# Performance work log

Measured on AMD Instinct MI355X. Metric: run time of the kernel, lower is better.

The kernel has to match this reference:

```python
import jax, jax.numpy as jnp
import numpy as np
import math

BS, QL, KL = 2, 2048, 2048
H, D = 16, 64          # n_heads, cell_dim
QS = KS = VS = 1024    # query/key/value feature sizes
HD = H * D


def setup_inputs() -> dict:
    key = jax.random.key(0)
    ks = jax.random.split(key, 12)
    s_in = 1.0 / math.sqrt(QS)
    s_hd = 1.0 / math.sqrt(HD)
    return {
        "query": jax.random.normal(ks[0], (BS, QL, QS), jnp.float32),
        "key": jax.random.normal(ks[1], (BS, KL, KS), jnp.float32),
        "value": jax.random.normal(ks[2], (BS, KL, VS), jnp.float32),
        # nn.Linear weights stored as [in, out] for x @ W + b
        "Wq_w": jax.random.normal(ks[3], (QS, HD), jnp.float32) * s_in,
        "Wq_b": jax.random.normal(ks[4], (HD,), jnp.float32) * s_in,
        "Wk_w": jax.random.normal(ks[5], (KS, HD), jnp.float32) * s_in,
        "Wk_b": jax.random.normal(ks[6], (HD,), jnp.float32) * s_in,
        "Wv_w": jax.random.normal(ks[7], (VS, HD), jnp.float32) * s_in,
        "Wv_b": jax.random.normal(ks[8], (HD,), jnp.float32) * s_in,
        "Wo_w": jax.random.normal(ks[9], (HD, HD), jnp.float32) * s_hd,
        "Wo_b": jax.random.normal(ks[10], (HD,), jnp.float32) * s_hd,
    }


def reference(query, key, value, Wq_w, Wq_b, Wk_w, Wk_b, Wv_w, Wv_b, Wo_w, Wo_b):
    bs, ql, _ = query.shape
    kl = key.shape[1]
    # project and split heads; torch .chunk along dim 2 == head-major reshape
    q = (query @ Wq_w + Wq_b).reshape(bs, ql, H, D).transpose(0, 2, 1, 3)  # bhqd
    k = (key @ Wk_w + Wk_b).reshape(bs, kl, H, D).transpose(0, 2, 1, 3)    # bhkd
    v = (value @ Wv_w + Wv_b).reshape(bs, kl, H, D).transpose(0, 2, 1, 3)  # bhkd
    scores = jnp.einsum("bhqd,bhkd->bhqk", q, k) / jnp.sqrt(jnp.float32(D))
    # log_softmax(...).exp() == softmax (use_mask=False path)
    w = jax.nn.softmax(scores, axis=-1)
    heads = jnp.einsum("bhqk,bhkd->bhqd", w, v)
    out = heads.transpose(0, 2, 1, 3).reshape(bs, ql, HD)  # concat heads on dim 2
    return out @ Wo_w + Wo_b
```

## Files before the change

kernel.cpp:

```cpp
#include <hip/hip_runtime.h>

#define BSZ 2
#define SEQ 2048
#define NH 16
#define DHD 64
#define HDIM 1024
#define FS 1024
#define MR (BSZ*SEQ)
#define L2E 1.4426950408889634f

typedef __bf16 bf16x8 __attribute__((ext_vector_type(8)));
typedef __bf16 bf16x2t __attribute__((ext_vector_type(2)));
typedef float f32x4 __attribute__((ext_vector_type(4)));
typedef float f32x16 __attribute__((ext_vector_type(16)));
typedef unsigned short u16;
typedef unsigned int u32;
typedef u32 u32x4 __attribute__((ext_vector_type(4)));

__device__ __forceinline__ u16 f2bf(float f) {
  u32 x = __float_as_uint(f);
  return (u16)((x + 0x7fffu + ((x >> 16) & 1u)) >> 16);
}

__device__ __forceinline__ u32 pack2bf(float a, float b) {
  bf16x2t t = {(__bf16)a, (__bf16)b};
  return __builtin_bit_cast(u32, t);
}

__device__ __forceinline__ void gload16(const void* g, void* l) {
  __builtin_amdgcn_global_load_lds(
      (const __attribute__((address_space(1))) u32*)g,
      (__attribute__((address_space(3))) u32*)l, 16, 0, 0);
}

__global__ __launch_bounds__(256) void cast3_k(const float* __restrict__ q,
                                               const float* __restrict__ k,
                                               const float* __restrict__ v,
                                               u16* __restrict__ dst, int n4) {
  int i = blockIdx.x * 256 + threadIdx.x;
  const int st = gridDim.x * 256;
  const int tot = 3 * n4;
  for (; i < tot; i += st) {
    const int arr = i >> 20;
    const int idx = i & (n4 - 1);
    const float* src = arr == 0 ? q : arr == 1 ? k : v;
    float4 vv = ((const float4*)src)[idx];
    ushort4 o;
    o.x = f2bf(vv.x); o.y = f2bf(vv.y); o.z = f2bf(vv.z); o.w = f2bf(vv.w);
    ((ushort4*)dst)[i] = o;
  }
}

__global__ __launch_bounds__(256) void transw4_k(
    const float* __restrict__ W0, const float* __restrict__ W1,
    const float* __restrict__ W2, const float* __restrict__ W3,
    u16* __restrict__ WTbase) {
  __shared__ float t[32][33];
  const int z = blockIdx.z;
  const float* W = z == 0 ? W0 : z == 1 ? W1 : z == 2 ? W2 : W3;
  u16* WT = WTbase + (size_t)z * FS * HDIM;
  const int tx = threadIdx.x, ty = threadIdx.y;
  const int c0 = blockIdx.x * 32, r0 = blockIdx.y * 32;
#pragma unroll
  for (int i = 0; i < 4; i++)
    t[ty + 8 * i][tx] = W[(size_t)(r0 + ty + 8 * i) * FS + c0 + tx];
  __syncthreads();
#pragma unroll
  for (int i = 0; i < 4; i++)
    WT[(size_t)(c0 + ty + 8 * i) * FS + r0 + tx] = f2bf(t[tx][ty + 8 * i]);
}

__global__ __launch_bounds__(256, 2) void gemmQKV_k(
    const u16* __restrict__ Abase, const u16* __restrict__ WTbase,
    const float* __restrict__ bq, const float* __restrict__ bk,
    const float* __restrict__ bv, u16* __restrict__ QKbase,
    u16* __restrict__ VpT) {
  __shared__ u16 aL[128 * 64];
  __shared__ u16 bL[128 * 64];
  const int grp = blockIdx.y;
  const u16* A = Abase + (size_t)grp * MR * FS;
  const u16* BT = WTbase + (size_t)grp * FS * HDIM;
  const float* bias = grp == 0 ? bq : grp == 1 ? bk : bv;
  const int m0 = (blockIdx.x >> 3) << 7;
  const int n0 = (blockIdx.x & 7) << 7;
  const int tid = threadIdx.x, w = tid >> 6, lane = tid & 63;
  const int wr = ((w >> 1) << 6), wc = ((w & 1) << 6);
  const int li = lane & 15, g = lane >> 4;

  f32x4 acc[4][4];
#pragma unroll
  for (int i = 0; i < 4; i++)
#pragma unroll
    for (int j = 0; j < 4; j++) acc[i][j] = (f32x4){0.f, 0.f, 0.f, 0.f};

  for (int k0 = 0; k0 < FS; k0 += 64) {
#pragma unroll
    for (int j = 0; j < 4; j++) {
      const int c = w * 4 + j;
      const int r = c * 8 + (lane >> 3);
      const int sc = (lane & 7) ^ (r & 7);
      gload16(A + (size_t)(m0 + r) * FS + k0 + sc * 8, (char*)aL + c * 1024);
      gload16(BT + (size_t)(n0 + r) * FS + k0 + sc * 8, (char*)bL + c * 1024);
    }
    __syncthreads();
    bf16x8 af[2][4], bfr[2][4];
#pragma unroll
    for (int ks = 0; ks < 2; ks++) {
#pragma unroll
      for (int mf = 0; mf < 4; mf++) {
        const int r = wr + mf * 16 + li;
        const int sl = (g + 4 * ks) ^ (r & 7);
        af[ks][mf] = *(const bf16x8*)((const char*)aL + r * 128 + sl * 16);
      }
#pragma unroll
      for (int nf = 0; nf < 4; nf++) {
        const int r = wc + nf * 16 + li;
        const int sl = (g + 4 * ks) ^ (r & 7);
        bfr[ks][nf] = *(const bf16x8*)((const char*)bL + r * 128 + sl * 16);
      }
    }
#pragma unroll
    for (int ks = 0; ks < 2; ks++)
#pragma unroll
      for (int mf = 0; mf < 4; mf++)
#pragma unroll
        for (int nf = 0; nf < 4; nf++)
          acc[mf][nf] = __builtin_amdgcn_mfma_f32_16x16x32_bf16(
              af[ks][mf], bfr[ks][nf], acc[mf][nf], 0, 0, 0);
    __syncthreads();
  }

  if (grp < 2) {
    const float osc = grp == 0 ? 0.125f * L2E : 1.0f;
    u16* C = QKbase + (size_t)grp * MR * HDIM;
#pragma unroll
    for (int mf = 0; mf < 4; mf++)
#pragma unroll
      for (int nf = 0; nf < 4; nf++) {
        const int n = n0 + wc + nf * 16 + li;
        const float bvl = bias[n];
#pragma unroll
        for (int r4 = 0; r4 < 4; r4++) {
          const int m = m0 + wr + mf * 16 + g * 4 + r4;
          C[(size_t)m * HDIM + n] = f2bf((acc[mf][nf][r4] + bvl) * osc);
        }
      }
  } else {
#pragma unroll
    for (int mf = 0; mf < 4; mf++)
#pragma unroll
      for (int nf = 0; nf < 4; nf++) {
        const int n = n0 + wc + nf * 16 + li;
        const float bvl = bias[n];
        const int m = m0 + wr + mf * 16 + g * 4;
        const int bb = m >> 11, kv = m & 2047;
        ushort4 o;
        o.x = f2bf(acc[mf][nf][0] + bvl);
        o.y = f2bf(acc[mf][nf][1] + bvl);
        o.z = f2bf(acc[mf][nf][2] + bvl);
        o.w = f2bf(acc[mf][nf][3] + bvl);
        *(ushort4*)(VpT +
                    ((size_t)(bb * NH + (n >> 6)) * DHD + (n & 63)) * SEQ + kv) = o;
      }
  }
}

__global__ __launch_bounds__(256, 2) void gemm_out_k(
    const u16* __restrict__ A, const u16* __restrict__ BT,
    const float* __restrict__ bias, float* __restrict__ C) {
  __shared__ u16 aL[128 * 64];
  __shared__ u16 bL[128 * 64];
  const int m0 = (blockIdx.x >> 3) << 7;
  const int n0 = (blockIdx.x & 7) << 7;
  const int tid = threadIdx.x, w = tid >> 6, lane = tid & 63;
  const int wr = ((w >> 1) << 6), wc = ((w & 1) << 6);
  const int li = lane & 15, g = lane >> 4;

  f32x4 acc[4][4];
#pragma unroll
  for (int i = 0; i < 4; i++)
#pragma unroll
    for (int j = 0; j < 4; j++) acc[i][j] = (f32x4){0.f, 0.f, 0.f, 0.f};

  for (int k0 = 0; k0 < HDIM; k0 += 64) {
#pragma unroll
    for (int j = 0; j < 4; j++) {
      const int c = w * 4 + j;
      const int r = c * 8 + (lane >> 3);
      const int sc = (lane & 7) ^ (r & 7);
      gload16(A + (size_t)(m0 + r) * HDIM + k0 + sc * 8, (char*)aL + c * 1024);
      gload16(BT + (size_t)(n0 + r) * HDIM + k0 + sc * 8, (char*)bL + c * 1024);
    }
    __syncthreads();
    bf16x8 af[2][4], bfr[2][4];
#pragma unroll
    for (int ks = 0; ks < 2; ks++) {
#pragma unroll
      for (int mf = 0; mf < 4; mf++) {
        const int r = wr + mf * 16 + li;
        const int sl = (g + 4 * ks) ^ (r & 7);
        af[ks][mf] = *(const bf16x8*)((const char*)aL + r * 128 + sl * 16);
      }
#pragma unroll
      for (int nf = 0; nf < 4; nf++) {
        const int r = wc + nf * 16 + li;
        const int sl = (g + 4 * ks) ^ (r & 7);
        bfr[ks][nf] = *(const bf16x8*)((const char*)bL + r * 128 + sl * 16);
      }
    }
#pragma unroll
    for (int ks = 0; ks < 2; ks++)
#pragma unroll
      for (int mf = 0; mf < 4; mf++)
#pragma unroll
        for (int nf = 0; nf < 4; nf++)
          acc[mf][nf] = __builtin_amdgcn_mfma_f32_16x16x32_bf16(
              af[ks][mf], bfr[ks][nf], acc[mf][nf], 0, 0, 0);
    __syncthreads();
  }

#pragma unroll
  for (int mf = 0; mf < 4; mf++)
#pragma unroll
    for (int nf = 0; nf < 4; nf++) {
      const int n = n0 + wc + nf * 16 + li;
      const float bvl = bias[n];
#pragma unroll
      for (int r4 = 0; r4 < 4; r4++) {
        const int m = m0 + wr + mf * 16 + g * 4 + r4;
        C[(size_t)m * HDIM + n] = acc[mf][nf][r4] + bvl;
      }
    }
}

__global__ __launch_bounds__(512, 1) void attn_k(
    const u16* __restrict__ Qp, const u16* __restrict__ Kp,
    const u16* __restrict__ VpT, u16* __restrict__ Hd) {
  __shared__ u16 kbuf[4][64 * 64];
  __shared__ u16 vbuf[4][64 * 64];

  const int bid = blockIdx.x;
  const int swz = (bid & 7) * 64 + (bid >> 3);
  const int qb = swz & 15;
  const int h = (swz >> 4) & 15;
  const int b = swz >> 8;
  const int tid = threadIdx.x, w = tid >> 6, lane = tid & 63;
  const int sel = w >> 2, g3 = w & 3;
  const int q32 = lane & 31, hi = lane >> 5;
  const int q0 = qb << 7;
  const size_t qbase = (size_t)(b * SEQ + q0) * HDIM + (size_t)h * DHD;
  const size_t kbase = (size_t)(b * SEQ) * HDIM + (size_t)h * DHD;
  const size_t vtbase = (size_t)(b * NH + h) * DHD * SEQ;

  const int rr = lane >> 3;
  const int sc8 = ((lane & 7) ^ rr) * 8;
  const int fkey = (q32 & 7) << 4;

#pragma unroll
  for (int j = 0; j < 2; j++) {
    const int c = w * 2 + j;
    const int r = c * 8 + rr;
    gload16(Qp + qbase + (size_t)r * HDIM + sc8, (char*)kbuf + c * 1024);
  }
  __syncthreads();
  bf16x8 qf[4];
  {
    const char* qbp = (const char*)kbuf + (g3 * 32 + q32) * 128;
#pragma unroll
    for (int ds = 0; ds < 4; ds++)
      qf[ds] = *(const bf16x8*)(qbp + ((32 * ds + 16 * hi) ^ fkey));
  }
  __syncthreads();

  float mrun = -1e30f, lrun = 0.f;
  f32x16 o0, o1;
#pragma unroll
  for (int i = 0; i < 16; i++) { o0[i] = 0.f; o1[i] = 0.f; }

  auto stagePair = [&](int tp) {
    const int t = tp + sel;
    const int buf = t & 3;
    const size_t kb = kbase + (size_t)(t * 64) * HDIM;
    const size_t vb = vtbase + (size_t)(t * 64);
#pragma unroll
    for (int j = 0; j < 2; j++) {
      const int c = g3 * 2 + j;
      const int r = c * 8 + rr;
      gload16(Kp + kb + (size_t)r * HDIM + sc8, (char*)kbuf[buf] + c * 1024);
      gload16(VpT + vb + (size_t)r * SEQ + sc8, (char*)vbuf[buf] + c * 1024);
    }
  };

  stagePair(0);

#pragma unroll 1
  for (int p = 0; p < SEQ / 128; p++) {
    __syncthreads();
    if (p + 1 < SEQ / 128) stagePair(2 * p + 2);
    const int t = 2 * p + sel;
    const char* kl = (const char*)kbuf[t & 3];
    const char* vl = (const char*)vbuf[t & 3];

    f32x16 s0, s1;
#pragma unroll
    for (int i = 0; i < 16; i++) { s0[i] = 0.f; s1[i] = 0.f; }
#pragma unroll
    for (int ds = 0; ds < 4; ds++) {
      const int off = (32 * ds + 16 * hi) ^ fkey;
      const bf16x8 ka = *(const bf16x8*)(kl + q32 * 128 + off);
      const bf16x8 kb2 = *(const bf16x8*)(kl + (32 + q32) * 128 + off);
      s0 = __builtin_amdgcn_mfma_f32_32x32x16_bf16(ka, qf[ds], s0, 0, 0, 0);
      s1 = __builtin_amdgcn_mfma_f32_32x32x16_bf16(kb2, qf[ds], s1, 0, 0, 0);
    }

    float mt[16];
#pragma unroll
    for (int i = 0; i < 16; i++) mt[i] = fmaxf(s0[i], s1[i]);
#pragma unroll
    for (int i = 0; i < 8; i++) mt[i] = fmaxf(mt[i], mt[i + 8]);
#pragma unroll
    for (int i = 0; i < 4; i++) mt[i] = fmaxf(mt[i], mt[i + 4]);
    float mx = fmaxf(fmaxf(mt[0], mt[1]), fmaxf(mt[2], mt[3]));
    mx = fmaxf(mx, __shfl_xor(mx, 32));
    if (!__all(mx <= mrun + 8.0f)) {
      const float mnew = fmaxf(mrun, mx);
      const float scl = __builtin_amdgcn_exp2f(mrun - mnew);
      mrun = mnew;
      lrun *= scl;
#pragma unroll
      for (int i = 0; i < 16; i++) { o0[i] *= scl; o1[i] *= scl; }
    }
    float p0[16], p1[16];
#pragma unroll
    for (int i = 0; i < 16; i++) {
      p0[i] = __builtin_amdgcn_exp2f(s0[i] - mrun);
      p1[i] = __builtin_amdgcn_exp2f(s1[i] - mrun);
    }
    float st[16];
#pragma unroll
    for (int i = 0; i < 16; i++) st[i] = p0[i] + p1[i];
#pragma unroll
    for (int i = 0; i < 8; i++) st[i] += st[i + 8];
#pragma unroll
    for (int i = 0; i < 4; i++) st[i] += st[i + 4];
    float rs = (st[0] + st[1]) + (st[2] + st[3]);
    rs += __shfl_xor(rs, 32);
    lrun += rs;

#pragma unroll
    for (int kvs = 0; kvs < 4; kvs++) {
      const float* ps = (kvs < 2) ? p0 : p1;
      const int rb = (kvs & 1) * 8;
      u32 w01 = pack2bf(ps[rb + 0], ps[rb + 1]);
      u32 w23 = pack2bf(ps[rb + 2], ps[rb + 3]);
      u32 w45 = pack2bf(ps[rb + 4], ps[rb + 5]);
      u32 w67 = pack2bf(ps[rb + 6], ps[rb + 7]);
      asm("v_permlane32_swap_b32 %0, %1" : "+v"(w01), "+v"(w45));
      asm("v_permlane32_swap_b32 %0, %1" : "+v"(w23), "+v"(w67));
      u32x4 uw = {w01, w23, w45, w67};
      const bf16x8 pf = __builtin_bit_cast(bf16x8, uw);
      const int off = (32 * kvs + 16 * hi) ^ fkey;
      const bf16x8 va = *(const bf16x8*)(vl + q32 * 128 + off);
      const bf16x8 vb2 = *(const bf16x8*)(vl + (32 + q32) * 128 + off);
      o0 = __builtin_amdgcn_mfma_f32_32x32x16_bf16(va, pf, o0, 0, 0, 0);
      o1 = __builtin_amdgcn_mfma_f32_32x32x16_bf16(vb2, pf, o1, 0, 0, 0);
    }
  }

  __syncthreads();
  char* mbase = (char*)kbuf + (g3 * 64 + lane) * 144;
  if (sel == 1) {
#pragma unroll
    for (int i = 0; i < 4; i++) {
      *(f32x4*)(mbase + i * 16) =
          (f32x4){o0[4 * i], o0[4 * i + 1], o0[4 * i + 2], o0[4 * i + 3]};
      *(f32x4*)(mbase + 64 + i * 16) =
          (f32x4){o1[4 * i], o1[4 * i + 1], o1[4 * i + 2], o1[4 * i + 3]};
    }
    *(float*)(mbase + 128) = mrun;
    *(float*)(mbase + 132) = lrun;
  }
  __syncthreads();
  if (sel == 0) {
    const float m2 = *(const float*)(mbase + 128);
    const float l2 = *(const float*)(mbase + 132);
    const float ms = fmaxf(mrun, m2);
    const float f1 = __builtin_amdgcn_exp2f(mrun - ms);
    const float f2 = __builtin_amdgcn_exp2f(m2 - ms);
    const float inv = 1.f / (lrun * f1 + l2 * f2);
    const int q = q0 + g3 * 32 + q32;
    u16* orow = Hd + (size_t)(b * SEQ + q) * HDIM + (size_t)h * DHD;
#pragma unroll
    for (int rg = 0; rg < 4; rg++) {
      const f32x4 a2 = *(const f32x4*)(mbase + rg * 16);
      const f32x4 b2 = *(const f32x4*)(mbase + 64 + rg * 16);
      ushort4 ov;
      ov.x = f2bf((o0[4 * rg + 0] * f1 + a2[0] * f2) * inv);
      ov.y = f2bf((o0[4 * rg + 1] * f1 + a2[1] * f2) * inv);
      ov.z = f2bf((o0[4 * rg + 2] * f1 + a2[2] * f2) * inv);
      ov.w = f2bf((o0[4 * rg + 3] * f1 + a2[3] * f2) * inv);
      *(ushort4*)(orow + 8 * rg + 4 * hi) = ov;
      ushort4 ow;
      ow.x = f2bf((o1[4 * rg + 0] * f1 + b2[0] * f2) * inv);
      ow.y = f2bf((o1[4 * rg + 1] * f1 + b2[1] * f2) * inv);
      ow.z = f2bf((o1[4 * rg + 2] * f1 + b2[2] * f2) * inv);
      ow.w = f2bf((o1[4 * rg + 3] * f1 + b2[3] * f2) * inv);
      *(ushort4*)(orow + 32 + 8 * rg + 4 * hi) = ow;
    }
  }
}

extern "C" void kernel_launch(void* const* d_in, const int* in_sizes, int n_in,
                              void* d_out, int out_size, void* d_ws, size_t ws_size,
                              hipStream_t stream) {
  (void)in_sizes; (void)n_in; (void)out_size; (void)ws_size;
  const float* q_in = (const float*)d_in[0];
  const float* k_in = (const float*)d_in[1];
  const float* v_in = (const float*)d_in[2];
  const float* Wq_w = (const float*)d_in[3];
  const float* Wq_b = (const float*)d_in[4];
  const float* Wk_w = (const float*)d_in[5];
  const float* Wk_b = (const float*)d_in[6];
  const float* Wv_w = (const float*)d_in[7];
  const float* Wv_b = (const float*)d_in[8];
  const float* Wo_w = (const float*)d_in[9];
  const float* Wo_b = (const float*)d_in[10];

  char* ws = (char*)d_ws;
  size_t off = 0;
  auto alloc = [&](size_t n) {
    char* p = ws + off;
    off += (n + 255) & ~(size_t)255;
    return p;
  };
  u16* qkv = (u16*)alloc((size_t)3 * MR * FS * 2);
  u16* wT = (u16*)alloc((size_t)4 * FS * HDIM * 2);
  u16* QK = (u16*)alloc((size_t)2 * MR * HDIM * 2);
  u16* VpT = (u16*)alloc((size_t)MR * HDIM * 2);
  u16* Hdp = (u16*)alloc((size_t)MR * HDIM * 2);

  const int n4 = MR * FS / 4;
  cast3_k<<<3072, 256, 0, stream>>>(q_in, k_in, v_in, qkv, n4);

  transw4_k<<<dim3(FS / 32, FS / 32, 4), dim3(32, 8), 0, stream>>>(
      Wq_w, Wk_w, Wv_w, Wo_w, wT);

  gemmQKV_k<<<dim3(256, 3), 256, 0, stream>>>(qkv, wT, Wq_b, Wk_b, Wv_b, QK,
                                              VpT);

  attn_k<<<BSZ * NH * (SEQ / 128), 512, 0, stream>>>(
      QK, QK + (size_t)MR * HDIM, VpT, Hdp);

  gemm_out_k<<<256, 256, 0, stream>>>(Hdp, wT + (size_t)3 * FS * HDIM, Wo_b,
                                      (float*)d_out);
}
```

Measured before the change: 126.6 us.

## Fuse fp32-to-bf16 input cast into QKV GEMM and simplify attention staging

Removes the separate cast kernel and its bf16 staging buffer. The QKV GEMM now reads fp32 activations directly, converts them to bf16 in registers and writes them to LDS, instead of using async global-to-LDS loads. The attention kernel's K/V staging replaces per-iteration address recomputation with incrementing pointers and a simpler double-buffer index. In exchange, the GEMM reads twice the bytes per A tile through synchronous vector loads, and each A tile is re-read by all 8 N-blocks, which may reduce load/compute overlap.

```diff
diff --git a/kernel.cpp b/kernel.cpp
--- a/kernel.cpp
+++ b/kernel.cpp
@@ -31,24 +31,6 @@
   __builtin_amdgcn_global_load_lds(
       (const __attribute__((address_space(1))) u32*)g,
       (__attribute__((address_space(3))) u32*)l, 16, 0, 0);
-}
-
-__global__ __launch_bounds__(256) void cast3_k(const float* __restrict__ q,
-                                               const float* __restrict__ k,
-                                               const float* __restrict__ v,
-                                               u16* __restrict__ dst, int n4) {
-  int i = blockIdx.x * 256 + threadIdx.x;
-  const int st = gridDim.x * 256;
-  const int tot = 3 * n4;
-  for (; i < tot; i += st) {
-    const int arr = i >> 20;
-    const int idx = i & (n4 - 1);
-    const float* src = arr == 0 ? q : arr == 1 ? k : v;
-    float4 vv = ((const float4*)src)[idx];
-    ushort4 o;
-    o.x = f2bf(vv.x); o.y = f2bf(vv.y); o.z = f2bf(vv.z); o.w = f2bf(vv.w);
-    ((ushort4*)dst)[i] = o;
-  }
 }
 
 __global__ __launch_bounds__(256) void transw4_k(
@@ -71,14 +53,15 @@
 }
 
 __global__ __launch_bounds__(256, 2) void gemmQKV_k(
-    const u16* __restrict__ Abase, const u16* __restrict__ WTbase,
+    const float* __restrict__ qf32, const float* __restrict__ kf32,
+    const float* __restrict__ vf32, const u16* __restrict__ WTbase,
     const float* __restrict__ bq, const float* __restrict__ bk,
     const float* __restrict__ bv, u16* __restrict__ QKbase,
     u16* __restrict__ VpT) {
   __shared__ u16 aL[128 * 64];
   __shared__ u16 bL[128 * 64];
   const int grp = blockIdx.y;
-  const u16* A = Abase + (size_t)grp * MR * FS;
+  const float* Af = grp == 0 ? qf32 : grp == 1 ? kf32 : vf32;
   const u16* BT = WTbase + (size_t)grp * FS * HDIM;
   const float* bias = grp == 0 ? bq : grp == 1 ? bk : bv;
   const int m0 = (blockIdx.x >> 3) << 7;
@@ -99,8 +82,22 @@
       const int c = w * 4 + j;
       const int r = c * 8 + (lane >> 3);
       const int sc = (lane & 7) ^ (r & 7);
-      gload16(A + (size_t)(m0 + r) * FS + k0 + sc * 8, (char*)aL + c * 1024);
       gload16(BT + (size_t)(n0 + r) * FS + k0 + sc * 8, (char*)bL + c * 1024);
+    }
+#pragma unroll
+    for (int j = 0; j < 4; j++) {
+      const int c = w * 4 + j;
+      const int r = c * 8 + (lane >> 3);
+      const int sc = (lane & 7) ^ (r & 7);
+      const float* src = Af + (size_t)(m0 + r) * FS + k0 + sc * 8;
+      const float4 a0 = *(const float4*)src;
+      const float4 a1 = *(const float4*)(src + 4);
+      u32x4 pk;
+      pk[0] = pack2bf(a0.x, a0.y);
+      pk[1] = pack2bf(a0.z, a0.w);
+      pk[2] = pack2bf(a1.x, a1.y);
+      pk[3] = pack2bf(a1.z, a1.w);
+      *(u32x4*)((char*)aL + c * 1024 + lane * 16) = pk;
     }
     __syncthreads();
     bf16x8 af[2][4], bfr[2][4];
@@ -277,29 +274,33 @@
 #pragma unroll
   for (int i = 0; i < 16; i++) { o0[i] = 0.f; o1[i] = 0.f; }
 
-  auto stagePair = [&](int tp) {
-    const int t = tp + sel;
-    const int buf = t & 3;
-    const size_t kb = kbase + (size_t)(t * 64) * HDIM;
-    const size_t vb = vtbase + (size_t)(t * 64);
-#pragma unroll
-    for (int j = 0; j < 2; j++) {
-      const int c = g3 * 2 + j;
-      const int r = c * 8 + rr;
-      gload16(Kp + kb + (size_t)r * HDIM + sc8, (char*)kbuf[buf] + c * 1024);
-      gload16(VpT + vb + (size_t)r * SEQ + sc8, (char*)vbuf[buf] + c * 1024);
-    }
+  const int c0j = g3 * 2;
+  const int r0r = c0j * 8 + rr;
+  const u16* kp0 = Kp + kbase + (size_t)(r0r + sel * 64) * HDIM + sc8;
+  const u16* kp1 = kp0 + (size_t)8 * HDIM;
+  const u16* vp0 = VpT + vtbase + (size_t)r0r * SEQ + sel * 64 + sc8;
+  const u16* vp1 = vp0 + (size_t)8 * SEQ;
+  const int ldk0 = c0j * 1024, ldk1 = (c0j + 1) * 1024;
+
+  auto stage2 = [&](int buf) {
+    gload16(kp0, (char*)kbuf[buf] + ldk0);
+    gload16(kp1, (char*)kbuf[buf] + ldk1);
+    gload16(vp0, (char*)vbuf[buf] + ldk0);
+    gload16(vp1, (char*)vbuf[buf] + ldk1);
+    kp0 += (size_t)128 * HDIM;
+    kp1 += (size_t)128 * HDIM;
+    vp0 += 128;
+    vp1 += 128;
   };
 
-  stagePair(0);
+  stage2(sel);
 
 #pragma unroll 1
   for (int p = 0; p < SEQ / 128; p++) {
     __syncthreads();
-    if (p + 1 < SEQ / 128) stagePair(2 * p + 2);
-    const int t = 2 * p + sel;
-    const char* kl = (const char*)kbuf[t & 3];
-    const char* vl = (const char*)vbuf[t & 3];
+    if (p + 1 < SEQ / 128) stage2(sel + 2 * ((p + 1) & 1));
+    const char* kl = (const char*)kbuf[sel + 2 * (p & 1)];
+    const char* vl = (const char*)vbuf[sel + 2 * (p & 1)];
 
     f32x16 s0, s1;
 #pragma unroll
@@ -433,20 +434,16 @@
     off += (n + 255) & ~(size_t)255;
     return p;
   };
-  u16* qkv = (u16*)alloc((size_t)3 * MR * FS * 2);
   u16* wT = (u16*)alloc((size_t)4 * FS * HDIM * 2);
   u16* QK = (u16*)alloc((size_t)2 * MR * HDIM * 2);
   u16* VpT = (u16*)alloc((size_t)MR * HDIM * 2);
   u16* Hdp = (u16*)alloc((size_t)MR * HDIM * 2);
 
-  const int n4 = MR * FS / 4;
-  cast3_k<<<3072, 256, 0, stream>>>(q_in, k_in, v_in, qkv, n4);
-
   transw4_k<<<dim3(FS / 32, FS / 32, 4), dim3(32, 8), 0, stream>>>(
       Wq_w, Wk_w, Wv_w, Wo_w, wT);
 
-  gemmQKV_k<<<dim3(256, 3), 256, 0, stream>>>(qkv, wT, Wq_b, Wk_b, Wv_b, QK,
-                                              VpT);
+  gemmQKV_k<<<dim3(256, 3), 256, 0, stream>>>(q_in, k_in, v_in, wT, Wq_b,
+                                              Wk_b, Wv_b, QK, VpT);
 
   attn_k<<<BSZ * NH * (SEQ / 128), 512, 0, stream>>>(
       QK, QK + (size_t)MR * HDIM, VpT, Hdp);
```

Result: slower. 148.1 us (+17.0%).
